# Optimization experiments

Measured on AMD Instinct MI355X. Metric: run time of the kernel, lower is better.

The kernel has to match this reference:

```python
import jax, jax.numpy as jnp
import numpy as np

EPS = 1e-12  # F.normalize eps


def _norm_adj(flow):
    # flow: (T, C, C). PyG gcn_norm with self-loops on the dense cosine-sim graph.
    T = flow.shape[0]
    x = flow.reshape(T, -1)                                  # (T, N)
    xn = x / jnp.clip(jnp.linalg.norm(x, axis=1, keepdims=True), EPS)
    A = xn.T @ xn                                            # (N, N) cosine sims
    N = A.shape[0]
    deg = A.sum(axis=0) + 1.0                                # +1 from added self-loop weight
    dinv = jnp.where(deg > 0, jax.lax.rsqrt(deg), 0.0)
    return (A + jnp.eye(N, dtype=A.dtype)) * dinv[:, None] * dinv[None, :]


def setup_inputs() -> dict:
    key = jax.random.key(0)
    ks = jax.random.split(key, 8)
    B, T, C, E = 8, 24, 64, 32
    H = 32
    O = 32
    return {
        "Flow": jax.random.normal(ks[0], (B, T, C, C), dtype=jnp.float32),
        "Edge": jax.random.normal(ks[1], (B, C, C, E), dtype=jnp.float32),
        "W0": jax.random.normal(ks[2], (E, H), dtype=jnp.float32) * 0.1,
        "b0": jax.random.normal(ks[3], (H,), dtype=jnp.float32) * 0.1,
        "W1": jax.random.normal(ks[4], (H, H), dtype=jnp.float32) * 0.1,
        "b1": jax.random.normal(ks[5], (H,), dtype=jnp.float32) * 0.1,
        "W2": jax.random.normal(ks[6], (H, O), dtype=jnp.float32) * 0.1,
        "b2": jax.random.normal(ks[7], (O,), dtype=jnp.float32) * 0.1,
    }


def reference(Flow, Edge, W0, b0, W1, b1, W2, b2):
    B, C, _, E = Edge.shape

    def per_batch(flow, edge):
        A = _norm_adj(flow)                                  # (N, N)
        x = edge.reshape(C * C, E)                           # (N, E)
        for W, b in ((W0, b0), (W1, b1), (W2, b2)):
            x = jax.nn.relu(A @ (x @ W) + b)
        return x.reshape(C, C, -1)

    return jax.vmap(per_batch)(Flow, Edge)                   # (B, C, C, out)
```

## Files before the change

kernel.cpp:

```cpp
#include <hip/hip_runtime.h>

#define BB 8
#define TT 24
#define NN 4096
#define HH 32
#define JT 64
#define UPB (TT*HH)

__global__ __launch_bounds__(256) void k_norm(const float* __restrict__ Flow,
                                              float* __restrict__ rn,
                                              float* __restrict__ s,
                                              float* __restrict__ u ) {
    int row = blockIdx.x;
    int tid = threadIdx.x;
    const float4* x = (const float4*)(Flow + (size_t)row * NN);
    float sq = 0.f, sm = 0.f;
#pragma unroll
    for (int i = 0; i < 4; ++i) {
        float4 v = x[tid + i * 256];
        sq += v.x * v.x + v.y * v.y + v.z * v.z + v.w * v.w;
        sm += v.x + v.y + v.z + v.w;
    }
#pragma unroll
    for (int off = 32; off > 0; off >>= 1) {
        sq += __shfl_down(sq, off);
        sm += __shfl_down(sm, off);
    }
    __shared__ float rss[4], rsm[4];
    int wave = tid >> 6, lane = tid & 63;
    if (lane == 0) { rss[wave] = sq; rsm[wave] = sm; }
    __syncthreads();
    if (tid == 0) {
        float tss = rss[0] + rss[1] + rss[2] + rss[3];
        float tsm = rsm[0] + rsm[1] + rsm[2] + rsm[3];
        float r = 1.0f / fmaxf(sqrtf(tss), 1e-12f);
        rn[row] = r;
        s[row] = tsm * r;
    }
    int gid = row * 256 + tid;
    if (gid < 3 * BB * TT * HH) u[gid] = 0.f;
}

__global__ __launch_bounds__(256) void k_dinvA0(const float* __restrict__ Flow,
                                                const float* __restrict__ Edge,
                                                const float* __restrict__ W0,
                                                const float* __restrict__ rn,
                                                const float* __restrict__ s,
                                                float* __restrict__ dinv,
                                                float* __restrict__ z0,
                                                float* __restrict__ u0) {
    const int blk = blockIdx.x;
    const int b = blk >> 6;
    const int j0 = (blk & 63) * JT;
    const int tid = threadIdx.x;

    __shared__ float xns[TT][JT];
    __shared__ float xs[JT][33];
    __shared__ float zs[JT][33];
    __shared__ float Ws[32][32];
    __shared__ float sS[TT];

    if (tid < TT) sS[tid] = s[b * TT + tid];
    for (int i = tid; i < 1024; i += 256) Ws[i >> 5][i & 31] = W0[i];
    {
        const float4* eb = (const float4*)(Edge + ((size_t)b * NN + j0) * HH);
#pragma unroll
        for (int k = 0; k < 2; ++k) {
            int i = tid + k * 256;
            float4 v = eb[i];
            int r0 = i >> 3, c0 = (i & 7) * 4;
            xs[r0][c0] = v.x; xs[r0][c0 + 1] = v.y; xs[r0][c0 + 2] = v.z; xs[r0][c0 + 3] = v.w;
        }
    }
    {
        const float* flb = Flow + (size_t)b * TT * NN + j0;
        for (int i = tid; i < TT * (JT / 4); i += 256) {
            int t = i >> 4, c0 = (i & 15) * 4;
            float4 v = ((const float4*)(flb + t * NN))[i & 15];
            float rt = rn[b * TT + t];
            xns[t][c0] = v.x * rt; xns[t][c0 + 1] = v.y * rt;
            xns[t][c0 + 2] = v.z * rt; xns[t][c0 + 3] = v.w * rt;
        }
    }
    __syncthreads();

    const int r = tid >> 2;
    const int h0 = (tid & 3) * 8;
    float deg = 1.0f;
#pragma unroll
    for (int t = 0; t < TT; ++t) deg += xns[t][r] * sS[t];
    const float di = (deg > 0.f) ? rsqrtf(deg) : 0.f;
    if ((tid & 3) == 0) dinv[b * NN + j0 + r] = di;

    float zr[8];
#pragma unroll
    for (int hh = 0; hh < 8; ++hh) {
        float acc = 0.f;
#pragma unroll
        for (int e = 0; e < 32; ++e) acc += xs[r][e] * Ws[e][h0 + hh];
        zr[hh] = di * acc;
        zs[r][h0 + hh] = zr[hh];
    }
    float* zb = z0 + ((size_t)b * NN + j0 + r) * HH + h0;
    ((float4*)zb)[0] = make_float4(zr[0], zr[1], zr[2], zr[3]);
    ((float4*)zb)[1] = make_float4(zr[4], zr[5], zr[6], zr[7]);
    __syncthreads();

#pragma unroll
    for (int k = 0; k < 3; ++k) {
        int p = tid + k * 256;
        int t = p >> 5, h = p & 31;
        float acc = 0.f;
#pragma unroll 8
        for (int rr = 0; rr < JT; ++rr) acc += xns[t][rr] * zs[rr][h];
        atomicAdd(&u0[(b * TT + t) * HH + h], acc);
    }
}

__global__ __launch_bounds__(256) void k_BA(const float* __restrict__ z_in,
                                            const float* __restrict__ Flow,
                                            const float* __restrict__ rn,
                                            const float* __restrict__ u_in,
                                            const float* __restrict__ dinv,
                                            const float* __restrict__ bias,
                                            const float* __restrict__ W,
                                            float* __restrict__ z_out,
                                            float* __restrict__ u_out) {
    const int blk = blockIdx.x;
    const int b = blk >> 6;
    const int j0 = (blk & 63) * JT;
    const int tid = threadIdx.x;

    __shared__ float us[TT][32];
    __shared__ float xns[TT][JT];
    __shared__ float Ws[32][32];
    __shared__ float xs[JT][33];
    __shared__ float zs[JT][33];
    __shared__ float bs[32];

    if (tid < 32) bs[tid] = bias[tid];
    for (int i = tid; i < 1024; i += 256) Ws[i >> 5][i & 31] = W[i];
    if (tid < UPB / 4) {
        float4 v = ((const float4*)(u_in + b * UPB))[tid];
        int t = tid >> 3, c0 = (tid & 7) * 4;
        us[t][c0] = v.x; us[t][c0 + 1] = v.y; us[t][c0 + 2] = v.z; us[t][c0 + 3] = v.w;
    }
    {
        const float* flb = Flow + (size_t)b * TT * NN + j0;
        for (int i = tid; i < TT * (JT / 4); i += 256) {
            int t = i >> 4, c0 = (i & 15) * 4;
            float4 v = ((const float4*)(flb + t * NN))[i & 15];
            float rt = rn[b * TT + t];
            xns[t][c0] = v.x * rt; xns[t][c0 + 1] = v.y * rt;
            xns[t][c0 + 2] = v.z * rt; xns[t][c0 + 3] = v.w * rt;
        }
    }
    const int r = tid >> 2;
    const int h0 = (tid & 3) * 8;
    const float di = dinv[b * NN + j0 + r];
    const float* zrow = z_in + ((size_t)b * NN + j0 + r) * HH + h0;
    float4 zv0 = ((const float4*)zrow)[0];
    float4 zv1 = ((const float4*)zrow)[1];
    __syncthreads();

    float zreg[8] = { zv0.x, zv0.y, zv0.z, zv0.w, zv1.x, zv1.y, zv1.z, zv1.w };
#pragma unroll
    for (int hh = 0; hh < 8; ++hh) {
        int h = h0 + hh;
        float acc = 0.f;
#pragma unroll
        for (int t = 0; t < TT; ++t) acc += xns[t][r] * us[t][h];
        xs[r][h] = fmaxf(di * (acc + zreg[hh]) + bs[h], 0.f);
    }
    float zr[8];
#pragma unroll
    for (int hh = 0; hh < 8; ++hh) {
        float acc = 0.f;
#pragma unroll
        for (int e = 0; e < 32; ++e) acc += xs[r][e] * Ws[e][h0 + hh];
        zr[hh] = di * acc;
        zs[r][h0 + hh] = zr[hh];
    }
    float* zb = z_out + ((size_t)b * NN + j0 + r) * HH + h0;
    ((float4*)zb)[0] = make_float4(zr[0], zr[1], zr[2], zr[3]);
    ((float4*)zb)[1] = make_float4(zr[4], zr[5], zr[6], zr[7]);
    __syncthreads();

#pragma unroll
    for (int k = 0; k < 3; ++k) {
        int p = tid + k * 256;
        int t = p >> 5, h = p & 31;
        float acc = 0.f;
#pragma unroll 8
        for (int rr = 0; rr < JT; ++rr) acc += xns[t][rr] * zs[rr][h];
        atomicAdd(&u_out[(b * TT + t) * HH + h], acc);
    }
}

__global__ __launch_bounds__(256) void k_Bfin(const float* __restrict__ z_in,
                                              const float* __restrict__ Flow,
                                              const float* __restrict__ rn,
                                              const float* __restrict__ u_in,
                                              const float* __restrict__ dinv,
                                              const float* __restrict__ bias,
                                              float* __restrict__ out) {
    const int blk = blockIdx.x;
    const int b = blk >> 6;
    const int j0 = (blk & 63) * JT;
    const int tid = threadIdx.x;

    __shared__ float us[TT][32];
    __shared__ float xns[TT][JT];
    __shared__ float bs[32];

    if (tid < 32) bs[tid] = bias[tid];
    if (tid < UPB / 4) {
        float4 v = ((const float4*)(u_in + b * UPB))[tid];
        int t = tid >> 3, c0 = (tid & 7) * 4;
        us[t][c0] = v.x; us[t][c0 + 1] = v.y; us[t][c0 + 2] = v.z; us[t][c0 + 3] = v.w;
    }
    {
        const float* flb = Flow + (size_t)b * TT * NN + j0;
        for (int i = tid; i < TT * (JT / 4); i += 256) {
            int t = i >> 4, c0 = (i & 15) * 4;
            float4 v = ((const float4*)(flb + t * NN))[i & 15];
            float rt = rn[b * TT + t];
            xns[t][c0] = v.x * rt; xns[t][c0 + 1] = v.y * rt;
            xns[t][c0 + 2] = v.z * rt; xns[t][c0 + 3] = v.w * rt;
        }
    }
    const int r = tid >> 2;
    const int h0 = (tid & 3) * 8;
    const float di = dinv[b * NN + j0 + r];
    const float* zrow = z_in + ((size_t)b * NN + j0 + r) * HH + h0;
    float4 zv0 = ((const float4*)zrow)[0];
    float4 zv1 = ((const float4*)zrow)[1];
    __syncthreads();

    float zreg[8] = { zv0.x, zv0.y, zv0.z, zv0.w, zv1.x, zv1.y, zv1.z, zv1.w };
    float o[8];
#pragma unroll
    for (int hh = 0; hh < 8; ++hh) {
        int h = h0 + hh;
        float acc = 0.f;
#pragma unroll
        for (int t = 0; t < TT; ++t) acc += xns[t][r] * us[t][h];
        o[hh] = fmaxf(di * (acc + zreg[hh]) + bs[h], 0.f);
    }
    float* orow = out + ((size_t)b * NN + j0 + r) * HH + h0;
    ((float4*)orow)[0] = make_float4(o[0], o[1], o[2], o[3]);
    ((float4*)orow)[1] = make_float4(o[4], o[5], o[6], o[7]);
}

extern "C" void kernel_launch(void* const* d_in, const int* in_sizes, int n_in,
                              void* d_out, int out_size, void* d_ws, size_t ws_size,
                              hipStream_t stream) {
    const float* Flow = (const float*)d_in[0];
    const float* Edge = (const float*)d_in[1];
    const float* W0 = (const float*)d_in[2];
    const float* b0 = (const float*)d_in[3];
    const float* W1 = (const float*)d_in[4];
    const float* b1 = (const float*)d_in[5];
    const float* W2 = (const float*)d_in[6];
    const float* b2 = (const float*)d_in[7];
    float* out = (float*)d_out;

    float* ws = (float*)d_ws;
    float* rn   = ws;
    float* s    = rn + BB * TT;
    float* dinv = s + BB * TT;
    float* zA   = dinv + (size_t)BB * NN;
    float* zB   = zA + (size_t)BB * NN * HH;
    float* u    = zB + (size_t)BB * NN * HH;
    float* u0 = u, *u1 = u + BB * TT * HH, *u2 = u + 2 * BB * TT * HH;

    k_norm<<<dim3(BB * TT), 256, 0, stream>>>(Flow, rn, s, u);
    k_dinvA0<<<dim3(512), 256, 0, stream>>>(Flow, Edge, W0, rn, s, dinv, zA, u0);
    k_BA<<<dim3(512), 256, 0, stream>>>(zA, Flow, rn, u0, dinv, b0, W1, zB, u1);
    k_BA<<<dim3(512), 256, 0, stream>>>(zB, Flow, rn, u1, dinv, b1, W2, zA, u2);
    k_Bfin<<<dim3(512), 256, 0, stream>>>(zA, Flow, rn, u2, dinv, b2, out);
}
```

Before: 46.34 us.

## Overlap row-norm reduction with Edge@W0 in a merged first kernel

Merges the row-norm kernel and the Edge@W0 matmul into one launch whose blocks split by index, so the independent W0 projection runs alongside the norm reduction. The projection is stored without the dinv scale, and dinv is applied later when z is read in the following kernels. The dinv/u0 kernel and the layer kernels now load raw z into shared memory and scale it there. This adds an extra read of z0raw in the dinv kernel, and the layer kernels now stage z through shared memory rather than registers.

```diff
diff --git a/kernel.cpp b/kernel.cpp
--- a/kernel.cpp
+++ b/kernel.cpp
@@ -7,47 +7,83 @@
 #define JT 64
 #define UPB (TT*HH)
 
-__global__ __launch_bounds__(256) void k_norm(const float* __restrict__ Flow,
-                                              float* __restrict__ rn,
-                                              float* __restrict__ s,
-                                              float* __restrict__ u ) {
-    int row = blockIdx.x;
-    int tid = threadIdx.x;
-    const float4* x = (const float4*)(Flow + (size_t)row * NN);
-    float sq = 0.f, sm = 0.f;
-#pragma unroll
-    for (int i = 0; i < 4; ++i) {
-        float4 v = x[tid + i * 256];
-        sq += v.x * v.x + v.y * v.y + v.z * v.z + v.w * v.w;
-        sm += v.x + v.y + v.z + v.w;
-    }
-#pragma unroll
-    for (int off = 32; off > 0; off >>= 1) {
-        sq += __shfl_down(sq, off);
-        sm += __shfl_down(sm, off);
-    }
-    __shared__ float rss[4], rsm[4];
-    int wave = tid >> 6, lane = tid & 63;
-    if (lane == 0) { rss[wave] = sq; rsm[wave] = sm; }
-    __syncthreads();
-    if (tid == 0) {
-        float tss = rss[0] + rss[1] + rss[2] + rss[3];
-        float tsm = rsm[0] + rsm[1] + rsm[2] + rsm[3];
-        float r = 1.0f / fmaxf(sqrtf(tss), 1e-12f);
-        rn[row] = r;
-        s[row] = tsm * r;
-    }
-    int gid = row * 256 + tid;
-    if (gid < 3 * BB * TT * HH) u[gid] = 0.f;
-}
-
-__global__ __launch_bounds__(256) void k_dinvA0(const float* __restrict__ Flow,
+__global__ __launch_bounds__(256) void k_phase1(const float* __restrict__ Flow,
                                                 const float* __restrict__ Edge,
                                                 const float* __restrict__ W0,
+                                                float* __restrict__ rn,
+                                                float* __restrict__ s,
+                                                float* __restrict__ u ,
+                                                float* __restrict__ z0raw) {
+    const int blk = blockIdx.x;
+    const int tid = threadIdx.x;
+
+    if (blk < BB * TT) {
+        const float4* x = (const float4*)(Flow + (size_t)blk * NN);
+        float sq = 0.f, sm = 0.f;
+#pragma unroll
+        for (int i = 0; i < 4; ++i) {
+            float4 v = x[tid + i * 256];
+            sq += v.x * v.x + v.y * v.y + v.z * v.z + v.w * v.w;
+            sm += v.x + v.y + v.z + v.w;
+        }
+#pragma unroll
+        for (int off = 32; off > 0; off >>= 1) {
+            sq += __shfl_down(sq, off);
+            sm += __shfl_down(sm, off);
+        }
+        __shared__ float rss[4], rsm[4];
+        int wave = tid >> 6, lane = tid & 63;
+        if (lane == 0) { rss[wave] = sq; rsm[wave] = sm; }
+        __syncthreads();
+        if (tid == 0) {
+            float tss = rss[0] + rss[1] + rss[2] + rss[3];
+            float tsm = rsm[0] + rsm[1] + rsm[2] + rsm[3];
+            float r = 1.0f / fmaxf(sqrtf(tss), 1e-12f);
+            rn[blk] = r;
+            s[blk] = tsm * r;
+        }
+        int gid = blk * 256 + tid;
+        if (gid < 3 * BB * TT * HH) u[gid] = 0.f;
+    } else {
+        const int g = blk - BB * TT;
+        const int b = g >> 6;
+        const int j0 = (g & 63) * JT;
+
+        __shared__ float xs[JT][33];
+        __shared__ float Ws[32][32];
+        for (int i = tid; i < 1024; i += 256) Ws[i >> 5][i & 31] = W0[i];
+        {
+            const float4* eb = (const float4*)(Edge + ((size_t)b * NN + j0) * HH);
+#pragma unroll
+            for (int k = 0; k < 2; ++k) {
+                int i = tid + k * 256;
+                float4 v = eb[i];
+                int r0 = i >> 3, c0 = (i & 7) * 4;
+                xs[r0][c0] = v.x; xs[r0][c0 + 1] = v.y; xs[r0][c0 + 2] = v.z; xs[r0][c0 + 3] = v.w;
+            }
+        }
+        __syncthreads();
+        const int r = tid >> 2;
+        const int h0 = (tid & 3) * 8;
+        float zr[8];
+#pragma unroll
+        for (int hh = 0; hh < 8; ++hh) {
+            float acc = 0.f;
+#pragma unroll
+            for (int e = 0; e < 32; ++e) acc += xs[r][e] * Ws[e][h0 + hh];
+            zr[hh] = acc;
+        }
+        float* zb = z0raw + ((size_t)b * NN + j0 + r) * HH + h0;
+        ((float4*)zb)[0] = make_float4(zr[0], zr[1], zr[2], zr[3]);
+        ((float4*)zb)[1] = make_float4(zr[4], zr[5], zr[6], zr[7]);
+    }
+}
+
+__global__ __launch_bounds__(256) void k_dinvU0(const float* __restrict__ Flow,
                                                 const float* __restrict__ rn,
                                                 const float* __restrict__ s,
+                                                const float* __restrict__ z0raw,
                                                 float* __restrict__ dinv,
-                                                float* __restrict__ z0,
                                                 float* __restrict__ u0) {
     const int blk = blockIdx.x;
     const int b = blk >> 6;
@@ -55,21 +91,18 @@
     const int tid = threadIdx.x;
 
     __shared__ float xns[TT][JT];
-    __shared__ float xs[JT][33];
     __shared__ float zs[JT][33];
-    __shared__ float Ws[32][32];
     __shared__ float sS[TT];
 
     if (tid < TT) sS[tid] = s[b * TT + tid];
-    for (int i = tid; i < 1024; i += 256) Ws[i >> 5][i & 31] = W0[i];
-    {
-        const float4* eb = (const float4*)(Edge + ((size_t)b * NN + j0) * HH);
+    {
+        const float4* zt = (const float4*)(z0raw + ((size_t)b * NN + j0) * HH);
 #pragma unroll
         for (int k = 0; k < 2; ++k) {
             int i = tid + k * 256;
-            float4 v = eb[i];
+            float4 v = zt[i];
             int r0 = i >> 3, c0 = (i & 7) * 4;
-            xs[r0][c0] = v.x; xs[r0][c0 + 1] = v.y; xs[r0][c0 + 2] = v.z; xs[r0][c0 + 3] = v.w;
+            zs[r0][c0] = v.x; zs[r0][c0 + 1] = v.y; zs[r0][c0 + 2] = v.z; zs[r0][c0 + 3] = v.w;
         }
     }
     {
@@ -91,19 +124,8 @@
     for (int t = 0; t < TT; ++t) deg += xns[t][r] * sS[t];
     const float di = (deg > 0.f) ? rsqrtf(deg) : 0.f;
     if ((tid & 3) == 0) dinv[b * NN + j0 + r] = di;
-
-    float zr[8];
-#pragma unroll
-    for (int hh = 0; hh < 8; ++hh) {
-        float acc = 0.f;
-#pragma unroll
-        for (int e = 0; e < 32; ++e) acc += xs[r][e] * Ws[e][h0 + hh];
-        zr[hh] = di * acc;
-        zs[r][h0 + hh] = zr[hh];
-    }
-    float* zb = z0 + ((size_t)b * NN + j0 + r) * HH + h0;
-    ((float4*)zb)[0] = make_float4(zr[0], zr[1], zr[2], zr[3]);
-    ((float4*)zb)[1] = make_float4(zr[4], zr[5], zr[6], zr[7]);
+#pragma unroll
+    for (int hh = 0; hh < 8; ++hh) zs[r][h0 + hh] *= di;
     __syncthreads();
 
 #pragma unroll
@@ -117,14 +139,14 @@
     }
 }
 
-__global__ __launch_bounds__(256) void k_BA(const float* __restrict__ z_in,
+__global__ __launch_bounds__(256) void k_BA(const float* __restrict__ zraw_in,
                                             const float* __restrict__ Flow,
                                             const float* __restrict__ rn,
                                             const float* __restrict__ u_in,
                                             const float* __restrict__ dinv,
                                             const float* __restrict__ bias,
                                             const float* __restrict__ W,
-                                            float* __restrict__ z_out,
+                                            float* __restrict__ zraw_out,
                                             float* __restrict__ u_out) {
     const int blk = blockIdx.x;
     const int b = blk >> 6;
@@ -144,6 +166,16 @@
         float4 v = ((const float4*)(u_in + b * UPB))[tid];
         int t = tid >> 3, c0 = (tid & 7) * 4;
         us[t][c0] = v.x; us[t][c0 + 1] = v.y; us[t][c0 + 2] = v.z; us[t][c0 + 3] = v.w;
+    }
+    {
+        const float4* zt = (const float4*)(zraw_in + ((size_t)b * NN + j0) * HH);
+#pragma unroll
+        for (int k = 0; k < 2; ++k) {
+            int i = tid + k * 256;
+            float4 v = zt[i];
+            int r0 = i >> 3, c0 = (i & 7) * 4;
+            zs[r0][c0] = v.x; zs[r0][c0 + 1] = v.y; zs[r0][c0 + 2] = v.z; zs[r0][c0 + 3] = v.w;
+        }
     }
     {
         const float* flb = Flow + (size_t)b * TT * NN + j0;
@@ -158,12 +190,11 @@
     const int r = tid >> 2;
     const int h0 = (tid & 3) * 8;
     const float di = dinv[b * NN + j0 + r];
-    const float* zrow = z_in + ((size_t)b * NN + j0 + r) * HH + h0;
-    float4 zv0 = ((const float4*)zrow)[0];
-    float4 zv1 = ((const float4*)zrow)[1];
-    __syncthreads();
-
-    float zreg[8] = { zv0.x, zv0.y, zv0.z, zv0.w, zv1.x, zv1.y, zv1.z, zv1.w };
+    __syncthreads();
+
+    float zreg[8];
+#pragma unroll
+    for (int hh = 0; hh < 8; ++hh) zreg[hh] = di * zs[r][h0 + hh];
 #pragma unroll
     for (int hh = 0; hh < 8; ++hh) {
         int h = h0 + hh;
@@ -178,10 +209,10 @@
         float acc = 0.f;
 #pragma unroll
         for (int e = 0; e < 32; ++e) acc += xs[r][e] * Ws[e][h0 + hh];
-        zr[hh] = di * acc;
-        zs[r][h0 + hh] = zr[hh];
-    }
-    float* zb = z_out + ((size_t)b * NN + j0 + r) * HH + h0;
+        zr[hh] = acc;
+        zs[r][h0 + hh] = di * zr[hh];
+    }
+    float* zb = zraw_out + ((size_t)b * NN + j0 + r) * HH + h0;
     ((float4*)zb)[0] = make_float4(zr[0], zr[1], zr[2], zr[3]);
     ((float4*)zb)[1] = make_float4(zr[4], zr[5], zr[6], zr[7]);
     __syncthreads();
@@ -197,7 +228,7 @@
     }
 }
 
-__global__ __launch_bounds__(256) void k_Bfin(const float* __restrict__ z_in,
+__global__ __launch_bounds__(256) void k_Bfin(const float* __restrict__ zraw_in,
                                               const float* __restrict__ Flow,
                                               const float* __restrict__ rn,
                                               const float* __restrict__ u_in,
@@ -232,12 +263,13 @@
     const int r = tid >> 2;
     const int h0 = (tid & 3) * 8;
     const float di = dinv[b * NN + j0 + r];
-    const float* zrow = z_in + ((size_t)b * NN + j0 + r) * HH + h0;
+    const float* zrow = zraw_in + ((size_t)b * NN + j0 + r) * HH + h0;
     float4 zv0 = ((const float4*)zrow)[0];
     float4 zv1 = ((const float4*)zrow)[1];
     __syncthreads();
 
-    float zreg[8] = { zv0.x, zv0.y, zv0.z, zv0.w, zv1.x, zv1.y, zv1.z, zv1.w };
+    float zreg[8] = { di * zv0.x, di * zv0.y, di * zv0.z, di * zv0.w,
+                      di * zv1.x, di * zv1.y, di * zv1.z, di * zv1.w };
     float o[8];
 #pragma unroll
     for (int hh = 0; hh < 8; ++hh) {
@@ -274,8 +306,8 @@
     float* u    = zB + (size_t)BB * NN * HH;
     float* u0 = u, *u1 = u + BB * TT * HH, *u2 = u + 2 * BB * TT * HH;
 
-    k_norm<<<dim3(BB * TT), 256, 0, stream>>>(Flow, rn, s, u);
-    k_dinvA0<<<dim3(512), 256, 0, stream>>>(Flow, Edge, W0, rn, s, dinv, zA, u0);
+    k_phase1<<<dim3(BB * TT + 512), 256, 0, stream>>>(Flow, Edge, W0, rn, s, u, zA);
+    k_dinvU0<<<dim3(512), 256, 0, stream>>>(Flow, rn, s, zA, dinv, u0);
     k_BA<<<dim3(512), 256, 0, stream>>>(zA, Flow, rn, u0, dinv, b0, W1, zB, u1);
     k_BA<<<dim3(512), 256, 0, stream>>>(zB, Flow, rn, u1, dinv, b1, W2, zA, u2);
     k_Bfin<<<dim3(512), 256, 0, stream>>>(zA, Flow, rn, u2, dinv, b2, out);
```

Result: faster. 43.07 us (-7.1%).
